# Kernel tuning notes

Hardware: AMD Instinct MI355X
Metric: run time of the kernel (lower is better)

The kernel has to match this reference:

```python
import jax, jax.numpy as jnp
import numpy as np

VOCAB = 65
N_EMBED = 384
BLOCK = 256
N_HEAD = 6
HEAD_SIZE = 4  # forward uses sa_heads = MultiHeadAttention(4), NOT the Block stack
B, T = 128, 256


def setup_inputs() -> dict:
    key = jax.random.key(0)
    ks = jax.random.split(key, 16)
    s = lambda *sh: 0.02
    inp = {
        "idx": jax.random.randint(ks[0], (B, T), 0, VOCAB),
        "targets": jax.random.randint(ks[1], (B, T), 0, VOCAB),
        "tok_emb": jax.random.normal(ks[2], (VOCAB, N_EMBED), jnp.float32) * 0.02,
        "pos_emb": jax.random.normal(ks[3], (BLOCK, N_EMBED), jnp.float32) * 0.02,
        "Wq": jax.random.normal(ks[4], (N_HEAD, N_EMBED, HEAD_SIZE), jnp.float32) * 0.05,
        "Wk": jax.random.normal(ks[5], (N_HEAD, N_EMBED, HEAD_SIZE), jnp.float32) * 0.05,
        "Wv": jax.random.normal(ks[6], (N_HEAD, N_EMBED, HEAD_SIZE), jnp.float32) * 0.05,
        "Wproj": jax.random.normal(ks[7], (N_HEAD * HEAD_SIZE, N_EMBED), jnp.float32) * 0.05,
        "bproj": jnp.zeros((N_EMBED,), jnp.float32),
        "W1": jax.random.normal(ks[8], (N_EMBED, 4 * N_EMBED), jnp.float32) * 0.02,
        "b1": jnp.zeros((4 * N_EMBED,), jnp.float32),
        "W2": jax.random.normal(ks[9], (4 * N_EMBED, N_EMBED), jnp.float32) * 0.02,
        "b2": jnp.zeros((N_EMBED,), jnp.float32),
        "Wlm": jax.random.normal(ks[10], (N_EMBED, VOCAB), jnp.float32) * 0.02,
        "blm": jnp.zeros((VOCAB,), jnp.float32),
    }
    return inp


def _forward(idx, targets, tok_emb, pos_emb, Wq, Wk, Wv, Wproj, bproj, W1, b1, W2, b2, Wlm, blm):
    Bb, Tt = idx.shape
    x = tok_emb[idx] + pos_emb[:Tt]  # [B,T,C]
    # multi-head attention (manual, causal). NOTE: source scales by n_embed**-0.5 (C of input), not head_size.
    q = jnp.einsum("btc,hcd->bhtd", x, Wq)
    k = jnp.einsum("btc,hcd->bhtd", x, Wk)
    v = jnp.einsum("btc,hcd->bhtd", x, Wv)
    scores = jnp.einsum("bhtd,bhsd->bhts", q, k) * (N_EMBED ** -0.5)
    causal = jnp.tril(jnp.ones((Tt, Tt), bool))
    scores = jnp.where(causal, scores, -jnp.inf)
    w = jax.nn.softmax(scores, axis=-1)  # dropout = identity in eval
    attn = jnp.einsum("bhts,bhsd->bhtd", w, v)
    attn = attn.transpose(0, 2, 1, 3).reshape(Bb, Tt, N_HEAD * HEAD_SIZE)
    x = attn @ Wproj + bproj
    # feed-forward
    x = jax.nn.relu(x @ W1 + b1) @ W2 + b2
    logits = x @ Wlm + blm  # [B,T,V]
    logits_flat = logits.reshape(Bb * Tt, VOCAB)
    t_flat = targets.reshape(Bb * Tt)
    logp = jax.nn.log_softmax(logits_flat, axis=-1)
    loss = -jnp.mean(jnp.take_along_axis(logp, t_flat[:, None], axis=1))
    return logits_flat, loss


def reference(idx, targets, tok_emb, pos_emb, Wq, Wk, Wv, Wproj, bproj, W1, b1, W2, b2, Wlm, blm):
    return _forward(idx, targets, tok_emb, pos_emb, Wq, Wk, Wv, Wproj, bproj, W1, b1, W2, b2, Wlm, blm)
```

## Files before the change

kernel.cpp:

```cpp
#include <hip/hip_runtime.h>
#include <hip/hip_bf16.h>
#include <math.h>

typedef __hip_bfloat16 bf16;
typedef __attribute__((ext_vector_type(8))) short bf16x8;
typedef __attribute__((ext_vector_type(4))) float f32x4;
typedef __attribute__((ext_vector_type(8))) int i32x8;
typedef __attribute__((ext_vector_type(4))) int i32x4;
typedef unsigned char u8;
typedef unsigned int u32;

#define T_SEQ   256
#define C_EMB   384
#define NH      6
#define HS      4
#define NB      128
#define NTOK    (NB * T_SEQ)
#define VOC     65
#define FFDIM   1536
#define QKVW    72
#define PROJK   32
#define XROWS   (VOC * T_SEQ)

#define X2_SCALE    128.0f
#define W1_SCALE    128.0f
#define FF1_DESCALE (1.0f / (128.0f * 128.0f))
#define H1_SCALE    512.0f
#define W2_SCALE    128.0f
#define FF2_DESCALE (1.0f / (512.0f * 128.0f))

__device__ __forceinline__ float b2f(bf16 x) { return __bfloat162float(x); }
__device__ __forceinline__ bf16  f2b(float x) { return __float2bfloat16(x); }
__device__ __forceinline__ short f2s(float x) { bf16 b = __float2bfloat16(x); return *reinterpret_cast<short*>(&b); }
__device__ __forceinline__ u8 f2fp8(float x) {
    return (u8)(__builtin_amdgcn_cvt_pk_fp8_f32(x, x, 0, false) & 0xff);
}
__device__ __forceinline__ u32 pk4fp8(const float* w) {
    int p = __builtin_amdgcn_cvt_pk_fp8_f32(w[0], w[1], 0, false);
    p = __builtin_amdgcn_cvt_pk_fp8_f32(w[2], w[3], p, true);
    return (u32)p;
}

__device__ __forceinline__ void glds16(const void* g, void* l) {
    __builtin_amdgcn_global_load_lds((const __attribute__((address_space(1))) void*)g,
                                     (__attribute__((address_space(3))) void*)l, 16, 0, 0);
}

__global__ void pack_all_kernel(const float* __restrict__ Wq, const float* __restrict__ Wk,
                                const float* __restrict__ Wv, const float* __restrict__ Wlm,
                                const float* __restrict__ Wproj,
                                const float* __restrict__ W1, const float* __restrict__ W2,
                                const float* __restrict__ tok_emb, const float* __restrict__ pos_emb,
                                bf16* __restrict__ WqkvT, bf16* __restrict__ WlmT,
                                bf16* __restrict__ WprojT, u8* __restrict__ W1f8,
                                u8* __restrict__ W2f8, bf16* __restrict__ xtab,
                                float* __restrict__ lossbuf) {
    int blk = blockIdx.x;
    if (blk == 0 && threadIdx.x == 0) { lossbuf[0] = 0.f; ((int*)lossbuf)[1] = 0; }
    if (blk < 128) {
        int n = blk;
        for (int c = threadIdx.x; c < C_EMB; c += 256) {
            float v = 0.f;
            if (n < QKVW) {
                int sel = n / 24, r = n % 24, h = r >> 2, d = r & 3;
                const float* W = (sel == 0) ? Wq : (sel == 1) ? Wk : Wv;
                v = W[(h * C_EMB + c) * HS + d];
            }
            WqkvT[(size_t)n * C_EMB + c] = f2b(v);
        }
    } else if (blk < 256) {
        int n = blk - 128;
        for (int c = threadIdx.x; c < C_EMB; c += 256)
            WlmT[(size_t)n * C_EMB + c] = f2b(n < VOC ? Wlm[(size_t)c * VOC + n] : 0.f);
    } else if (blk < 640) {
        int n = blk - 256;
        int k = threadIdx.x;
        if (k < PROJK)
            WprojT[(size_t)n * PROJK + k] = f2b(k < 24 ? Wproj[(size_t)k * C_EMB + n] : 0.f);
    } else if (blk < 640 + FFDIM) {
        int n = blk - 640;
        for (int k = threadIdx.x; k < C_EMB; k += 256)
            W1f8[(size_t)n * C_EMB + k] = f2fp8(W1[(size_t)k * FFDIM + n] * W1_SCALE);
    } else if (blk < 640 + FFDIM + C_EMB) {
        int n = blk - 640 - FFDIM;
        for (int k = threadIdx.x; k < FFDIM; k += 256)
            W2f8[(size_t)n * FFDIM + k] = f2fp8(W2[(size_t)k * C_EMB + n] * W2_SCALE);
    } else {
        int base = (blk - (640 + FFDIM + C_EMB)) * 4;
        for (int r = 0; r < 4; ++r) {
            int row = base + r;
            int id = row >> 8, t = row & 255;
            const float* te = tok_emb + (size_t)id * C_EMB;
            const float* pe = pos_emb + (size_t)t * C_EMB;
            bf16* dst = xtab + (size_t)row * C_EMB;
            for (int c = threadIdx.x; c < C_EMB; c += 256)
                dst[c] = f2b(te[c] + pe[c]);
        }
    }
}

__global__ __launch_bounds__(512)
void qkv_gather_kernel(const int* __restrict__ idx, const bf16* __restrict__ xtab,
                       const bf16* __restrict__ Bt, float* __restrict__ outf) {
    __shared__ __align__(16) u8 As[16384];
    __shared__ __align__(16) u8 Bs[16384];
    __shared__ int rowid[128];
    int tid = threadIdx.x, lane = tid & 63, wave = tid >> 6;
    int bm = blockIdx.x * 128;
    int wm = (wave & 1) * 64, wn = (wave >> 1) * 32;
    int lrow = lane & 15, kq = lane >> 4;
    if (tid < 128) { int token = bm + tid; rowid[tid] = idx[token] * T_SEQ + (token & (T_SEQ - 1)); }
    __syncthreads();

    int r0 = tid >> 3;
    int s0 = (((tid & 7) * 16) - (r0 & 7) * 16) & 127;
    int c1 = tid + 512;
    int r1 = c1 >> 3;
    int s1 = (((c1 & 7) * 16) - (r1 & 7) * 16) & 127;
    const u8* xb = (const u8*)xtab;
    const u8* bb = (const u8*)Bt;
    long gA0 = (long)rowid[r0] * 768 + s0;
    long gA1 = (long)rowid[r1] * 768 + s1;
    long gB0 = (long)r0 * 768 + s0;
    long gB1 = (long)r1 * 768 + s1;
    int ro = (lrow & 7) * 16;

    f32x4 acc[4][2] = {};
    for (int k0 = 0; k0 < 768; k0 += 128) {
        glds16(xb + gA0 + k0, As + (size_t)tid * 16);
        glds16(xb + gA1 + k0, As + (size_t)c1 * 16);
        glds16(bb + gB0 + k0, Bs + (size_t)tid * 16);
        glds16(bb + gB1 + k0, Bs + (size_t)c1 * 16);
        __syncthreads();
        #pragma unroll
        for (int ks = 0; ks < 2; ++ks) {
            int off = (ks * 64 + kq * 16 + ro) & 127;
            bf16x8 af[4], bff[2];
            #pragma unroll
            for (int i = 0; i < 4; ++i)
                af[i] = *(const bf16x8*)&As[(size_t)(wm + i * 16 + lrow) * 128 + off];
            #pragma unroll
            for (int i = 0; i < 2; ++i)
                bff[i] = *(const bf16x8*)&Bs[(size_t)(wn + i * 16 + lrow) * 128 + off];
            #pragma unroll
            for (int mi = 0; mi < 4; ++mi)
                #pragma unroll
                for (int ni = 0; ni < 2; ++ni)
                    acc[mi][ni] = __builtin_amdgcn_mfma_f32_16x16x32_bf16(af[mi], bff[ni], acc[mi][ni], 0, 0, 0);
        }
        __syncthreads();
    }

    #pragma unroll
    for (int ni = 0; ni < 2; ++ni) {
        int col = wn + ni * 16 + lrow;
        if (col >= QKVW) continue;
        #pragma unroll
        for (int mi = 0; mi < 4; ++mi) {
            int orow = bm + wm + mi * 16 + kq * 4;
            #pragma unroll
            for (int r = 0; r < 4; ++r)
                outf[(size_t)(orow + r) * QKVW + col] = acc[mi][ni][r];
        }
    }
}

__global__ void attn_kernel(const float* __restrict__ qkv,
                            bf16* __restrict__ attnT) {
    int bh = blockIdx.x;
    int b = bh / NH, h = bh % NH;
    int t = threadIdx.x;
    __shared__ float4 kv[T_SEQ][2];
    const float* base = qkv + (size_t)(b * T_SEQ) * QKVW;
    kv[t][0] = *(const float4*)(base + t * QKVW + 24 + h * HS);
    kv[t][1] = *(const float4*)(base + t * QKVW + 48 + h * HS);
    __syncthreads();
    const float scale = 0.05103103630798288f;
    float4 q = *(const float4*)(base + t * QKVW + h * HS);
    float qx = q.x * scale, qy = q.y * scale, qz = q.z * scale, qw = q.w * scale;
    float sum0 = 0.f, sum1 = 0.f;
    float o0x = 0.f, o0y = 0.f, o0z = 0.f, o0w = 0.f;
    float o1x = 0.f, o1y = 0.f, o1z = 0.f, o1w = 0.f;
    int s = 0;
    for (; s + 1 <= t; s += 2) {
        float4 k0 = kv[s][0],     v0 = kv[s][1];
        float4 k1 = kv[s + 1][0], v1 = kv[s + 1][1];
        float p0 = __expf(qx * k0.x + qy * k0.y + qz * k0.z + qw * k0.w);
        float p1 = __expf(qx * k1.x + qy * k1.y + qz * k1.z + qw * k1.w);
        sum0 += p0; sum1 += p1;
        o0x += p0 * v0.x; o0y += p0 * v0.y; o0z += p0 * v0.z; o0w += p0 * v0.w;
        o1x += p1 * v1.x; o1y += p1 * v1.y; o1z += p1 * v1.z; o1w += p1 * v1.w;
    }
    if (s <= t) {
        float4 k0 = kv[s][0], v0 = kv[s][1];
        float p0 = __expf(qx * k0.x + qy * k0.y + qz * k0.z + qw * k0.w);
        sum0 += p0;
        o0x += p0 * v0.x; o0y += p0 * v0.y; o0z += p0 * v0.z; o0w += p0 * v0.w;
    }
    float inv = 1.f / (sum0 + sum1);
    bf16* out = attnT + (size_t)(b * T_SEQ + t) * PROJK + h * HS;
    out[0] = f2b((o0x + o1x) * inv);
    out[1] = f2b((o0y + o1y) * inv);
    out[2] = f2b((o0z + o1z) * inv);
    out[3] = f2b((o0w + o1w) * inv);
    if (h == 0) {
        bf16* pad = attnT + (size_t)(b * T_SEQ + t) * PROJK + 24;
        *(uint4*)pad = uint4{0, 0, 0, 0};
    }
}

__global__ __launch_bounds__(256)
void gemm_mfma32_kernel(const bf16* __restrict__ A, const bf16* __restrict__ Bt,
                        const float* __restrict__ bias,
                        u8* __restrict__ outf8, float oscale,
                        int M, int K, int Nout) {
    __shared__ short As[128][32];
    __shared__ short Bs[128][32];
    int tid  = threadIdx.x;
    int lane = tid & 63;
    int wave = tid >> 6;
    int bm = blockIdx.y * 128;
    int bn = blockIdx.x * 128;
    int wm = (wave & 1) * 64;
    int wn = (wave >> 1) * 64;
    int lrow  = lane & 15;
    int khalf = lane >> 4;
    int arot = ((lrow >> 1) & 3) * 16;
    int roff = ((khalf * 16 + arot) & 63) >> 1;

    f32x4 acc[4][4] = {};
    for (int k0 = 0; k0 < K; k0 += 32) {
        #pragma unroll
        for (int h = 0; h < 2; ++h) {
            int c = tid + h * 256;
            int row = c >> 2;
            int i0 = (c & 3) * 16;
            int selem = ((i0 - ((row >> 1) & 3) * 16) & 63) >> 1;
            glds16(A  + (size_t)(bm + row) * K + k0 + selem, (short*)As + (size_t)c * 8);
            glds16(Bt + (size_t)(bn + row) * K + k0 + selem, (short*)Bs + (size_t)c * 8);
        }
        __syncthreads();

        bf16x8 af[4], bff[4];
        #pragma unroll
        for (int i = 0; i < 4; ++i) {
            af[i]  = *(const bf16x8*)&As[wm + i * 16 + lrow][roff];
            bff[i] = *(const bf16x8*)&Bs[wn + i * 16 + lrow][roff];
        }
        #pragma unroll
        for (int mi = 0; mi < 4; ++mi)
            #pragma unroll
            for (int ni = 0; ni < 4; ++ni)
                acc[mi][ni] = __builtin_amdgcn_mfma_f32_16x16x32_bf16(af[mi], bff[ni], acc[mi][ni], 0, 0, 0);
        __syncthreads();
    }

    #pragma unroll
    for (int ni = 0; ni < 4; ++ni) {
        int col = bn + wn + ni * 16 + lrow;
        float bv = bias[col];
        #pragma unroll
        for (int mi = 0; mi < 4; ++mi) {
            int row = bm + wm + mi * 16 + khalf * 4;
            float w[4];
            #pragma unroll
            for (int r = 0; r < 4; ++r) w[r] = (acc[mi][ni][r] + bv) * oscale;
            int p01 = __builtin_amdgcn_cvt_pk_fp8_f32(w[0], w[1], 0, false);
            int p23 = __builtin_amdgcn_cvt_pk_fp8_f32(w[2], w[3], 0, false);
            outf8[(size_t)(row + 0) * Nout + col] = (u8)(p01 & 0xff);
            outf8[(size_t)(row + 1) * Nout + col] = (u8)((p01 >> 8) & 0xff);
            outf8[(size_t)(row + 2) * Nout + col] = (u8)(p23 & 0xff);
            outf8[(size_t)(row + 3) * Nout + col] = (u8)((p23 >> 8) & 0xff);
        }
    }
}

__global__ __launch_bounds__(512)
void gemm_fp8_kernel(const u8* __restrict__ A, const u8* __restrict__ Bt,
                     const float* __restrict__ bias,
                     bf16* __restrict__ outb, u8* __restrict__ outf8,
                     float descale, float oscale,
                     int M, int K, int Nout, int NT, int relu) {
    __shared__ u8 smem[32768];
    u8* As = smem;
    u8* Bs = smem + 16384;
    int lin  = blockIdx.x;
    int xcd  = lin & 7;
    int loc  = lin >> 3;
    int nt   = loc % NT;
    int mloc = loc / NT;
    int MPX  = (M / 128) >> 3;
    int bm = (xcd * MPX + mloc) * 128;
    int bn = nt * 128;

    int tid  = threadIdx.x;
    int lane = tid & 63;
    int wave = tid >> 6;
    int wm = (wave & 1) * 64;
    int wn = (wave >> 1) * 32;
    int lrow  = lane & 15;
    int khalf = lane >> 4;

    f32x4 acc[4][2] = {};
    int r0 = tid >> 3;
    int i0 = (tid & 7) * 16;
    int s0 = (i0 - (r0 & 7) * 16) & 127;
    int arot = (lrow & 7) * 16;
    int off0 = (khalf * 32 + arot) & 127;
    int off1 = (off0 + 16) & 127;

    for (int k0 = 0; k0 < K; k0 += 128) {
        const u8* Ag = A  + (size_t)(bm + r0) * K + k0 + s0;
        const u8* Bg = Bt + (size_t)(bn + r0) * K + k0 + s0;
        glds16(Ag,                  As + (size_t)tid * 16);
        glds16(Ag + (size_t)64 * K, As + 8192 + (size_t)tid * 16);
        glds16(Bg,                  Bs + (size_t)tid * 16);
        glds16(Bg + (size_t)64 * K, Bs + 8192 + (size_t)tid * 16);
        __syncthreads();

        i32x8 a[4], b[2];
        #pragma unroll
        for (int i = 0; i < 4; ++i) {
            const u8* rp = As + (size_t)(wm + i * 16 + lrow) * 128;
            i32x4 lo = *(const i32x4*)(rp + off0);
            i32x4 hi = *(const i32x4*)(rp + off1);
            a[i][0]=lo[0]; a[i][1]=lo[1]; a[i][2]=lo[2]; a[i][3]=lo[3];
            a[i][4]=hi[0]; a[i][5]=hi[1]; a[i][6]=hi[2]; a[i][7]=hi[3];
        }
        #pragma unroll
        for (int i = 0; i < 2; ++i) {
            const u8* rp = Bs + (size_t)(wn + i * 16 + lrow) * 128;
            i32x4 lo = *(const i32x4*)(rp + off0);
            i32x4 hi = *(const i32x4*)(rp + off1);
            b[i][0]=lo[0]; b[i][1]=lo[1]; b[i][2]=lo[2]; b[i][3]=lo[3];
            b[i][4]=hi[0]; b[i][5]=hi[1]; b[i][6]=hi[2]; b[i][7]=hi[3];
        }
        #pragma unroll
        for (int mi = 0; mi < 4; ++mi)
            #pragma unroll
            for (int ni = 0; ni < 2; ++ni)
                acc[mi][ni] = __builtin_amdgcn_mfma_scale_f32_16x16x128_f8f6f4(
                    b[ni], a[mi], acc[mi][ni], 0, 0,
                    0, 0x7f7f7f7f, 0, 0x7f7f7f7f);
        __syncthreads();
    }

    if (outf8) {
        #pragma unroll
        for (int mi = 0; mi < 4; ++mi) {
            int m = wm + mi * 16 + lrow;
            #pragma unroll
            for (int ni = 0; ni < 2; ++ni) {
                int n0 = wn + ni * 16 + khalf * 4;
                float4 bv = *(const float4*)(bias + bn + n0);
                float w[4];
                w[0] = acc[mi][ni][0] * descale + bv.x;
                w[1] = acc[mi][ni][1] * descale + bv.y;
                w[2] = acc[mi][ni][2] * descale + bv.z;
                w[3] = acc[mi][ni][3] * descale + bv.w;
                if (relu) {
                    w[0] = fmaxf(w[0], 0.f); w[1] = fmaxf(w[1], 0.f);
                    w[2] = fmaxf(w[2], 0.f); w[3] = fmaxf(w[3], 0.f);
                }
                w[0] *= oscale; w[1] *= oscale; w[2] *= oscale; w[3] *= oscale;
                *(u32*)&smem[(size_t)m * 128 + ((n0 + (m & 7) * 16) & 127)] = pk4fp8(w);
            }
        }
        __syncthreads();
        #pragma unroll
        for (int p = 0; p < 2; ++p) {
            int c = tid + p * 512;
            int row = c >> 3;
            int g0 = (c & 7) * 16;
            uint4 v = *(const uint4*)&smem[(size_t)row * 128 + ((g0 + (row & 7) * 16) & 127)];
            *(uint4*)&outf8[(size_t)(bm + row) * Nout + bn + g0] = v;
        }
    } else {
        short* Es = (short*)smem;
        #pragma unroll
        for (int mi = 0; mi < 4; ++mi) {
            int m = wm + mi * 16 + lrow;
            #pragma unroll
            for (int ni = 0; ni < 2; ++ni) {
                int n0 = wn + ni * 16 + khalf * 4;
                float4 bv = *(const float4*)(bias + bn + n0);
                union { short s[4]; uint2 u; } pk;
                pk.s[0] = f2s(acc[mi][ni][0] * descale + bv.x);
                pk.s[1] = f2s(acc[mi][ni][1] * descale + bv.y);
                pk.s[2] = f2s(acc[mi][ni][2] * descale + bv.z);
                pk.s[3] = f2s(acc[mi][ni][3] * descale + bv.w);
                *(uint2*)&Es[(size_t)m * 128 + ((n0 + (m & 7) * 8) & 127)] = pk.u;
            }
        }
        __syncthreads();
        #pragma unroll
        for (int p = 0; p < 4; ++p) {
            int c = tid + p * 512;
            int row = c >> 4;
            int g0 = (c & 15) * 16;
            uint4 v = *(const uint4*)&smem[(size_t)row * 256 + ((g0 + (row & 7) * 16) & 255)];
            *(uint4*)((u8*)outb + ((size_t)(bm + row) * Nout + bn) * 2 + g0) = v;
        }
    }
}

__global__ __launch_bounds__(512)
void lm_loss_kernel(const bf16* __restrict__ A, const bf16* __restrict__ Bt,
                    const float* __restrict__ bias, const int* __restrict__ targets,
                    float* __restrict__ outf, float* __restrict__ lossbuf,
                    float* __restrict__ out_loss, int M, int K) {
    __shared__ short As[128][32];
    __shared__ short Bs[128][32];
    __shared__ float Ls[128][66];
    __shared__ float red[128];
    int tid  = threadIdx.x;
    int lane = tid & 63;
    int wave = tid >> 6;
    int bm = blockIdx.x * 128;
    int wm = (wave & 1) * 64;
    int wn = (wave >> 1) * 32;
    int lrow  = lane & 15;
    int khalf = lane >> 4;

    int row = tid >> 2;
    int i0 = (tid & 3) * 16;
    int selem = ((i0 - ((row >> 1) & 3) * 16) & 63) >> 1;
    int arot = ((lrow >> 1) & 3) * 16;
    int roff = ((khalf * 16 + arot) & 63) >> 1;

    f32x4 acc[4][2] = {};
    for (int k0 = 0; k0 < K; k0 += 32) {
        glds16(A  + (size_t)(bm + row) * K + k0 + selem, (short*)As + (size_t)tid * 8);
        glds16(Bt + (size_t)row * K + k0 + selem,        (short*)Bs + (size_t)tid * 8);
        __syncthreads();

        bf16x8 af[4], bff[2];
        #pragma unroll
        for (int i = 0; i < 4; ++i)
            af[i] = *(const bf16x8*)&As[wm + i * 16 + lrow][roff];
        #pragma unroll
        for (int i = 0; i < 2; ++i)
            bff[i] = *(const bf16x8*)&Bs[wn + i * 16 + lrow][roff];
        #pragma unroll
        for (int mi = 0; mi < 4; ++mi)
            #pragma unroll
            for (int ni = 0; ni < 2; ++ni)
                acc[mi][ni] = __builtin_amdgcn_mfma_f32_16x16x32_bf16(af[mi], bff[ni], acc[mi][ni], 0, 0, 0);
        __syncthreads();
    }

    #pragma unroll
    for (int ni = 0; ni < 2; ++ni) {
        int col = wn + ni * 16 + lrow;
        if (col >= VOC) continue;
        float bv = bias[col];
        #pragma unroll
        for (int mi = 0; mi < 4; ++mi) {
            int lr = wm + mi * 16 + khalf * 4;
            #pragma unroll
            for (int r = 0; r < 4; ++r) {
                float v = acc[mi][ni][r] + bv;
                outf[(size_t)(bm + lr + r) * VOC + col] = v;
                Ls[lr + r][col] = v;
            }
        }
    }
    __syncthreads();

    if (tid < 128) {
        int token = bm + tid;
        int tgt = targets[token];
        float m = -1e30f, s = 0.f;
        #pragma unroll 8
        for (int c = 0; c < VOC; ++c) {
            float v = Ls[tid][c];
            float mn = fmaxf(m, v);
            s = s * __expf(m - mn) + __expf(v - mn);
            m = mn;
        }
        red[tid] = m + logf(s) - Ls[tid][tgt];
    }
    __syncthreads();
    if (tid < 64) {
        float s = red[tid] + red[tid + 64];
        #pragma unroll
        for (int off = 32; off > 0; off >>= 1) s += __shfl_xor(s, off);
        if (tid == 0) {
            atomicAdd(&lossbuf[0], s);
            __threadfence();
            int done = atomicAdd(&((int*)lossbuf)[1], 1);
            if (done == (NTOK / 128) - 1) {
                __threadfence();
                float total = atomicAdd(&lossbuf[0], 0.0f);
                out_loss[0] = total / (float)NTOK;
            }
        }
    }
}

extern "C" void kernel_launch(void* const* d_in, const int* in_sizes, int n_in,
                              void* d_out, int out_size, void* d_ws, size_t ws_size,
                              hipStream_t stream) {
    const int*   idx     = (const int*)  d_in[0];
    const int*   targets = (const int*)  d_in[1];
    const float* tok_emb = (const float*)d_in[2];
    const float* pos_emb = (const float*)d_in[3];
    const float* Wq      = (const float*)d_in[4];
    const float* Wk      = (const float*)d_in[5];
    const float* Wv      = (const float*)d_in[6];
    const float* Wproj   = (const float*)d_in[7];
    const float* bproj   = (const float*)d_in[8];
    const float* W1      = (const float*)d_in[9];
    const float* b1      = (const float*)d_in[10];
    const float* W2      = (const float*)d_in[11];
    const float* b2      = (const float*)d_in[12];
    const float* Wlm     = (const float*)d_in[13];
    const float* blm     = (const float*)d_in[14];

    char* ws = (char*)d_ws;
    bf16*  WprojT = (bf16*) (ws + 0);
    float* qkvbuf = (float*)(ws + 25165824);
    bf16*  attnT  = (bf16*) (ws + 34603008);
    bf16*  xtab   = (bf16*) (ws + 37748736);
    u8*    h1f8   = (u8*)   (ws + 62914560);
    u8*    x2f8   = (u8*)   (ws + 113246208);
    bf16*  x3     = (bf16*) (ws + 163577856);
    float* lossbuf= (float*)(ws + 188743680);
    u8*    W1f8   = (u8*)   (ws + 188874752);
    u8*    W2f8   = (u8*)   (ws + 190054400);
    bf16*  WqkvT  = (bf16*) (ws + 191234048);
    bf16*  WlmT   = (bf16*) (ws + 191332352);

    float* out_logits = (float*)d_out;
    float* out_loss   = out_logits + (size_t)NTOK * VOC;

    pack_all_kernel<<<640 + FFDIM + C_EMB + XROWS / 4, 256, 0, stream>>>(
        Wq, Wk, Wv, Wlm, Wproj, W1, W2, tok_emb, pos_emb,
        WqkvT, WlmT, WprojT, W1f8, W2f8, xtab, lossbuf);

    qkv_gather_kernel<<<NTOK / 128, 512, 0, stream>>>(idx, xtab, WqkvT, qkvbuf);
    attn_kernel<<<NB * NH, T_SEQ, 0, stream>>>(qkvbuf, attnT);

    gemm_mfma32_kernel<<<dim3(C_EMB / 128, NTOK / 128), 256, 0, stream>>>(attnT, WprojT, bproj,
                                                                          x2f8, X2_SCALE,
                                                                          NTOK, PROJK, C_EMB);
    gemm_fp8_kernel<<<(NTOK / 128) * (FFDIM / 128), 512, 0, stream>>>(x2f8, W1f8, b1,
                                                                      nullptr, h1f8,
                                                                      FF1_DESCALE, H1_SCALE,
                                                                      NTOK, C_EMB, FFDIM, FFDIM / 128, 1);
    gemm_fp8_kernel<<<(NTOK / 128) * (C_EMB / 128), 512, 0, stream>>>(h1f8, W2f8, b2,
                                                                      x3, nullptr,
                                                                      FF2_DESCALE, 1.0f,
                                                                      NTOK, FFDIM, C_EMB, C_EMB / 128, 0);
    lm_loss_kernel<<<NTOK / 128, 512, 0, stream>>>(x3, WlmT, blm, targets,
                                                   out_logits, lossbuf, out_loss, NTOK, C_EMB);
}
```

Measured before the change: 228.3 us.

## Fuse projection, FF1 and FF2 GEMMs into one per-tile kernel

New measurement: 210.0 us. 8.0% less time.

```diff
diff --git a/kernel.cpp b/kernel.cpp
--- a/kernel.cpp
+++ b/kernel.cpp
@@ -29,7 +29,7 @@
 #define W2_SCALE    128.0f
 #define FF2_DESCALE (1.0f / (512.0f * 128.0f))
 
-__device__ __forceinline__ float b2f(bf16 x) { return __bfloat162float(x); }
+__device__ __forceinline__ float bf2f(bf16 x) { return __bfloat162float(x); }
 __device__ __forceinline__ bf16  f2b(float x) { return __float2bfloat16(x); }
 __device__ __forceinline__ short f2s(float x) { bf16 b = __float2bfloat16(x); return *reinterpret_cast<short*>(&b); }
 __device__ __forceinline__ u8 f2fp8(float x) {
@@ -209,198 +209,232 @@
     }
 }
 
-__global__ __launch_bounds__(256)
-void gemm_mfma32_kernel(const bf16* __restrict__ A, const bf16* __restrict__ Bt,
-                        const float* __restrict__ bias,
-                        u8* __restrict__ outf8, float oscale,
-                        int M, int K, int Nout) {
-    __shared__ short As[128][32];
-    __shared__ short Bs[128][32];
+__global__ __launch_bounds__(512, 2)
+void ff_mega_kernel(const bf16* __restrict__ attnT, const bf16* __restrict__ WprojT,
+                    const float* __restrict__ bproj,
+                    const u8* __restrict__ W1f8, const float* __restrict__ b1,
+                    const u8* __restrict__ W2f8, const float* __restrict__ b2,
+                    bf16* __restrict__ x3) {
+    __shared__ __align__(16) u8 smem[147456];
+    u8* x2_lds = smem;
+    u8* bs1    = smem + 49152;
+    u8* h1t    = smem + 81920;
+    u8* bs2    = smem + 98304;
+    short* As_p = (short*)(smem + 49152);
+    short* Bs_p = (short*)(smem + 57344);
+
     int tid  = threadIdx.x;
     int lane = tid & 63;
     int wave = tid >> 6;
-    int bm = blockIdx.y * 128;
-    int bn = blockIdx.x * 128;
-    int wm = (wave & 1) * 64;
-    int wn = (wave >> 1) * 64;
+    int bm   = blockIdx.x * 128;
+    int wm   = (wave & 1) * 64;
     int lrow  = lane & 15;
     int khalf = lane >> 4;
-    int arot = ((lrow >> 1) & 3) * 16;
-    int roff = ((khalf * 16 + arot) & 63) >> 1;
-
-    f32x4 acc[4][4] = {};
-    for (int k0 = 0; k0 < K; k0 += 32) {
-        #pragma unroll
-        for (int h = 0; h < 2; ++h) {
-            int c = tid + h * 256;
-            int row = c >> 2;
-            int i0 = (c & 3) * 16;
-            int selem = ((i0 - ((row >> 1) & 3) * 16) & 63) >> 1;
-            glds16(A  + (size_t)(bm + row) * K + k0 + selem, (short*)As + (size_t)c * 8);
-            glds16(Bt + (size_t)(bn + row) * K + k0 + selem, (short*)Bs + (size_t)c * 8);
-        }
-        __syncthreads();
-
-        bf16x8 af[4], bff[4];
-        #pragma unroll
-        for (int i = 0; i < 4; ++i) {
-            af[i]  = *(const bf16x8*)&As[wm + i * 16 + lrow][roff];
-            bff[i] = *(const bf16x8*)&Bs[wn + i * 16 + lrow][roff];
-        }
+
+    {
+        int row = tid >> 2;
+        int i0 = (tid & 3) * 16;
+        int selem = ((i0 - ((row >> 1) & 3) * 16) & 63) >> 1;
+        glds16(attnT + (size_t)(bm + row) * PROJK + selem, As_p + (size_t)tid * 8);
+        #pragma unroll
+        for (int p = 0; p < 3; ++p) {
+            int c = tid + p * 512;
+            int rowb = c >> 2;
+            int sel2 = (((c & 3) * 16 - ((rowb >> 1) & 3) * 16) & 63) >> 1;
+            glds16(WprojT + (size_t)rowb * PROJK + sel2, Bs_p + (size_t)c * 8);
+        }
+    }
+    __syncthreads();
+
+    int wn6 = (wave >> 1) * 96;
+    f32x4 accp[4][6] = {};
+    {
+        int arot16 = ((lrow >> 1) & 3) * 16;
+        int roff = ((khalf * 16 + arot16) & 63) >> 1;
+        bf16x8 afp[4], bfp[6];
+        #pragma unroll
+        for (int i = 0; i < 4; ++i)
+            afp[i] = *(const bf16x8*)&As_p[(size_t)(wm + i * 16 + lrow) * 32 + roff];
+        #pragma unroll
+        for (int i = 0; i < 6; ++i)
+            bfp[i] = *(const bf16x8*)&Bs_p[(size_t)(wn6 + i * 16 + lrow) * 32 + roff];
         #pragma unroll
         for (int mi = 0; mi < 4; ++mi)
             #pragma unroll
-            for (int ni = 0; ni < 4; ++ni)
-                acc[mi][ni] = __builtin_amdgcn_mfma_f32_16x16x32_bf16(af[mi], bff[ni], acc[mi][ni], 0, 0, 0);
-        __syncthreads();
+            for (int ni = 0; ni < 6; ++ni)
+                accp[mi][ni] = __builtin_amdgcn_mfma_f32_16x16x32_bf16(bfp[ni], afp[mi], accp[mi][ni], 0, 0, 0);
+    }
+    __syncthreads();
+
+    int r0 = tid >> 3;
+    int s0 = (((tid & 7) * 16) - (r0 & 7) * 16) & 127;
+
+    {
+        const u8* g = W1f8 + (size_t)r0 * 384 + s0;
+        glds16(g, bs1 + (size_t)tid * 16);
+        glds16(g + (size_t)64 * 384, bs1 + 8192 + (size_t)tid * 16);
+        const u8* g2 = W2f8 + (size_t)r0 * 1536 + s0;
+        #pragma unroll
+        for (int j = 0; j < 6; ++j)
+            glds16(g2 + (size_t)j * 64 * 1536, bs2 + (size_t)j * 8192 + (size_t)tid * 16);
     }
 
     #pragma unroll
-    for (int ni = 0; ni < 4; ++ni) {
-        int col = bn + wn + ni * 16 + lrow;
-        float bv = bias[col];
-        #pragma unroll
-        for (int mi = 0; mi < 4; ++mi) {
-            int row = bm + wm + mi * 16 + khalf * 4;
+    for (int mi = 0; mi < 4; ++mi) {
+        int m = wm + mi * 16 + lrow;
+        #pragma unroll
+        for (int ni = 0; ni < 6; ++ni) {
+            int n0 = wn6 + ni * 16 + khalf * 4;
+            float4 bv = *(const float4*)(bproj + n0);
             float w[4];
-            #pragma unroll
-            for (int r = 0; r < 4; ++r) w[r] = (acc[mi][ni][r] + bv) * oscale;
-            int p01 = __builtin_amdgcn_cvt_pk_fp8_f32(w[0], w[1], 0, false);
-            int p23 = __builtin_amdgcn_cvt_pk_fp8_f32(w[2], w[3], 0, false);
-            outf8[(size_t)(row + 0) * Nout + col] = (u8)(p01 & 0xff);
-            outf8[(size_t)(row + 1) * Nout + col] = (u8)((p01 >> 8) & 0xff);
-            outf8[(size_t)(row + 2) * Nout + col] = (u8)(p23 & 0xff);
-            outf8[(size_t)(row + 3) * Nout + col] = (u8)((p23 >> 8) & 0xff);
-        }
-    }
-}
-
-__global__ __launch_bounds__(512)
-void gemm_fp8_kernel(const u8* __restrict__ A, const u8* __restrict__ Bt,
-                     const float* __restrict__ bias,
-                     bf16* __restrict__ outb, u8* __restrict__ outf8,
-                     float descale, float oscale,
-                     int M, int K, int Nout, int NT, int relu) {
-    __shared__ u8 smem[32768];
-    u8* As = smem;
-    u8* Bs = smem + 16384;
-    int lin  = blockIdx.x;
-    int xcd  = lin & 7;
-    int loc  = lin >> 3;
-    int nt   = loc % NT;
-    int mloc = loc / NT;
-    int MPX  = (M / 128) >> 3;
-    int bm = (xcd * MPX + mloc) * 128;
-    int bn = nt * 128;
-
-    int tid  = threadIdx.x;
-    int lane = tid & 63;
-    int wave = tid >> 6;
-    int wm = (wave & 1) * 64;
-    int wn = (wave >> 1) * 32;
-    int lrow  = lane & 15;
-    int khalf = lane >> 4;
-
-    f32x4 acc[4][2] = {};
-    int r0 = tid >> 3;
-    int i0 = (tid & 7) * 16;
-    int s0 = (i0 - (r0 & 7) * 16) & 127;
-    int arot = (lrow & 7) * 16;
-    int off0 = (khalf * 32 + arot) & 127;
+            w[0] = (accp[mi][ni][0] + bv.x) * X2_SCALE;
+            w[1] = (accp[mi][ni][1] + bv.y) * X2_SCALE;
+            w[2] = (accp[mi][ni][2] + bv.z) * X2_SCALE;
+            w[3] = (accp[mi][ni][3] + bv.w) * X2_SCALE;
+            *(u32*)&x2_lds[(size_t)(n0 >> 7) * 16384 + (size_t)m * 128 +
+                           (((n0 & 127) + (m & 7) * 16) & 127)] = pk4fp8(w);
+        }
+    }
+    __syncthreads();
+
+    int arot8 = (lrow & 7) * 16;
+    int off0 = (khalf * 32 + arot8) & 127;
     int off1 = (off0 + 16) & 127;
-
-    for (int k0 = 0; k0 < K; k0 += 128) {
-        const u8* Ag = A  + (size_t)(bm + r0) * K + k0 + s0;
-        const u8* Bg = Bt + (size_t)(bn + r0) * K + k0 + s0;
-        glds16(Ag,                  As + (size_t)tid * 16);
-        glds16(Ag + (size_t)64 * K, As + 8192 + (size_t)tid * 16);
-        glds16(Bg,                  Bs + (size_t)tid * 16);
-        glds16(Bg + (size_t)64 * K, Bs + 8192 + (size_t)tid * 16);
-        __syncthreads();
-
-        i32x8 a[4], b[2];
-        #pragma unroll
-        for (int i = 0; i < 4; ++i) {
-            const u8* rp = As + (size_t)(wm + i * 16 + lrow) * 128;
-            i32x4 lo = *(const i32x4*)(rp + off0);
-            i32x4 hi = *(const i32x4*)(rp + off1);
-            a[i][0]=lo[0]; a[i][1]=lo[1]; a[i][2]=lo[2]; a[i][3]=lo[3];
-            a[i][4]=hi[0]; a[i][5]=hi[1]; a[i][6]=hi[2]; a[i][7]=hi[3];
-        }
-        #pragma unroll
-        for (int i = 0; i < 2; ++i) {
-            const u8* rp = Bs + (size_t)(wn + i * 16 + lrow) * 128;
-            i32x4 lo = *(const i32x4*)(rp + off0);
-            i32x4 hi = *(const i32x4*)(rp + off1);
-            b[i][0]=lo[0]; b[i][1]=lo[1]; b[i][2]=lo[2]; b[i][3]=lo[3];
-            b[i][4]=hi[0]; b[i][5]=hi[1]; b[i][6]=hi[2]; b[i][7]=hi[3];
-        }
-        #pragma unroll
-        for (int mi = 0; mi < 4; ++mi)
-            #pragma unroll
-            for (int ni = 0; ni < 2; ++ni)
-                acc[mi][ni] = __builtin_amdgcn_mfma_scale_f32_16x16x128_f8f6f4(
-                    b[ni], a[mi], acc[mi][ni], 0, 0,
-                    0, 0x7f7f7f7f, 0, 0x7f7f7f7f);
-        __syncthreads();
-    }
-
-    if (outf8) {
+    int wn2 = (wave >> 1) * 32;
+
+    f32x4 acc1[4][2] = {};
+    f32x4 acc2[4][6] = {};
+
+    for (int nt = 0; nt < 12; ++nt) {
+        #pragma unroll
+        for (int kk = 0; kk < 3; ++kk) {
+            int stp = nt * 3 + kk;
+            int cur = stp & 1;
+            int nxt = stp + 1;
+            if (nxt < 36) {
+                int nnt = nxt / 3, nk0 = (nxt % 3) * 128;
+                const u8* g = W1f8 + (size_t)(nnt * 128 + r0) * 384 + nk0 + s0;
+                u8* dst = bs1 + (size_t)(nxt & 1) * 16384;
+                glds16(g, dst + (size_t)tid * 16);
+                glds16(g + (size_t)64 * 384, dst + 8192 + (size_t)tid * 16);
+            }
+            const u8* abase = x2_lds + (size_t)kk * 16384;
+            const u8* bbase = bs1 + (size_t)cur * 16384;
+            i32x8 a[4], b[2];
+            #pragma unroll
+            for (int i = 0; i < 4; ++i) {
+                const u8* rp = abase + (size_t)(wm + i * 16 + lrow) * 128;
+                i32x4 lo = *(const i32x4*)(rp + off0);
+                i32x4 hi = *(const i32x4*)(rp + off1);
+                a[i][0]=lo[0]; a[i][1]=lo[1]; a[i][2]=lo[2]; a[i][3]=lo[3];
+                a[i][4]=hi[0]; a[i][5]=hi[1]; a[i][6]=hi[2]; a[i][7]=hi[3];
+            }
+            #pragma unroll
+            for (int i = 0; i < 2; ++i) {
+                const u8* rp = bbase + (size_t)(wn2 + i * 16 + lrow) * 128;
+                i32x4 lo = *(const i32x4*)(rp + off0);
+                i32x4 hi = *(const i32x4*)(rp + off1);
+                b[i][0]=lo[0]; b[i][1]=lo[1]; b[i][2]=lo[2]; b[i][3]=lo[3];
+                b[i][4]=hi[0]; b[i][5]=hi[1]; b[i][6]=hi[2]; b[i][7]=hi[3];
+            }
+            #pragma unroll
+            for (int mi = 0; mi < 4; ++mi)
+                #pragma unroll
+                for (int ni = 0; ni < 2; ++ni)
+                    acc1[mi][ni] = __builtin_amdgcn_mfma_scale_f32_16x16x128_f8f6f4(
+                        b[ni], a[mi], acc1[mi][ni], 0, 0,
+                        0, 0x7f7f7f7f, 0, 0x7f7f7f7f);
+            __syncthreads();
+        }
+
         #pragma unroll
         for (int mi = 0; mi < 4; ++mi) {
             int m = wm + mi * 16 + lrow;
             #pragma unroll
             for (int ni = 0; ni < 2; ++ni) {
-                int n0 = wn + ni * 16 + khalf * 4;
-                float4 bv = *(const float4*)(bias + bn + n0);
+                int n0 = wn2 + ni * 16 + khalf * 4;
+                float4 bv = *(const float4*)(b1 + nt * 128 + n0);
                 float w[4];
-                w[0] = acc[mi][ni][0] * descale + bv.x;
-                w[1] = acc[mi][ni][1] * descale + bv.y;
-                w[2] = acc[mi][ni][2] * descale + bv.z;
-                w[3] = acc[mi][ni][3] * descale + bv.w;
-                if (relu) {
-                    w[0] = fmaxf(w[0], 0.f); w[1] = fmaxf(w[1], 0.f);
-                    w[2] = fmaxf(w[2], 0.f); w[3] = fmaxf(w[3], 0.f);
+                w[0] = fmaxf(acc1[mi][ni][0] * FF1_DESCALE + bv.x, 0.f) * H1_SCALE;
+                w[1] = fmaxf(acc1[mi][ni][1] * FF1_DESCALE + bv.y, 0.f) * H1_SCALE;
+                w[2] = fmaxf(acc1[mi][ni][2] * FF1_DESCALE + bv.z, 0.f) * H1_SCALE;
+                w[3] = fmaxf(acc1[mi][ni][3] * FF1_DESCALE + bv.w, 0.f) * H1_SCALE;
+                *(u32*)&h1t[(size_t)m * 128 + ((n0 + (m & 7) * 16) & 127)] = pk4fp8(w);
+                acc1[mi][ni] = f32x4{0.f, 0.f, 0.f, 0.f};
+            }
+        }
+        __syncthreads();
+
+        {
+            i32x8 a2[4];
+            #pragma unroll
+            for (int i = 0; i < 4; ++i) {
+                const u8* rp = h1t + (size_t)(wm + i * 16 + lrow) * 128;
+                i32x4 lo = *(const i32x4*)(rp + off0);
+                i32x4 hi = *(const i32x4*)(rp + off1);
+                a2[i][0]=lo[0]; a2[i][1]=lo[1]; a2[i][2]=lo[2]; a2[i][3]=lo[3];
+                a2[i][4]=hi[0]; a2[i][5]=hi[1]; a2[i][6]=hi[2]; a2[i][7]=hi[3];
+            }
+            #pragma unroll
+            for (int half = 0; half < 2; ++half) {
+                i32x8 bw[3];
+                #pragma unroll
+                for (int j = 0; j < 3; ++j) {
+                    int ni = half * 3 + j;
+                    const u8* rp = bs2 + (size_t)(wn6 + ni * 16 + lrow) * 128;
+                    i32x4 lo = *(const i32x4*)(rp + off0);
+                    i32x4 hi = *(const i32x4*)(rp + off1);
+                    bw[j][0]=lo[0]; bw[j][1]=lo[1]; bw[j][2]=lo[2]; bw[j][3]=lo[3];
+                    bw[j][4]=hi[0]; bw[j][5]=hi[1]; bw[j][6]=hi[2]; bw[j][7]=hi[3];
                 }
-                w[0] *= oscale; w[1] *= oscale; w[2] *= oscale; w[3] *= oscale;
-                *(u32*)&smem[(size_t)m * 128 + ((n0 + (m & 7) * 16) & 127)] = pk4fp8(w);
+                #pragma unroll
+                for (int mi = 0; mi < 4; ++mi)
+                    #pragma unroll
+                    for (int j = 0; j < 3; ++j)
+                        acc2[mi][half * 3 + j] = __builtin_amdgcn_mfma_scale_f32_16x16x128_f8f6f4(
+                            bw[j], a2[mi], acc2[mi][half * 3 + j], 0, 0,
+                            0, 0x7f7f7f7f, 0, 0x7f7f7f7f);
             }
         }
         __syncthreads();
-        #pragma unroll
-        for (int p = 0; p < 2; ++p) {
-            int c = tid + p * 512;
-            int row = c >> 3;
-            int g0 = (c & 7) * 16;
-            uint4 v = *(const uint4*)&smem[(size_t)row * 128 + ((g0 + (row & 7) * 16) & 127)];
-            *(uint4*)&outf8[(size_t)(bm + row) * Nout + bn + g0] = v;
-        }
-    } else {
-        short* Es = (short*)smem;
-        #pragma unroll
-        for (int mi = 0; mi < 4; ++mi) {
-            int m = wm + mi * 16 + lrow;
-            #pragma unroll
-            for (int ni = 0; ni < 2; ++ni) {
-                int n0 = wn + ni * 16 + khalf * 4;
-                float4 bv = *(const float4*)(bias + bn + n0);
-                union { short s[4]; uint2 u; } pk;
-                pk.s[0] = f2s(acc[mi][ni][0] * descale + bv.x);
-                pk.s[1] = f2s(acc[mi][ni][1] * descale + bv.y);
-                pk.s[2] = f2s(acc[mi][ni][2] * descale + bv.z);
-                pk.s[3] = f2s(acc[mi][ni][3] * descale + bv.w);
-                *(uint2*)&Es[(size_t)m * 128 + ((n0 + (m & 7) * 8) & 127)] = pk.u;
-            }
-        }
-        __syncthreads();
-        #pragma unroll
-        for (int p = 0; p < 4; ++p) {
-            int c = tid + p * 512;
-            int row = c >> 4;
-            int g0 = (c & 15) * 16;
-            uint4 v = *(const uint4*)&smem[(size_t)row * 256 + ((g0 + (row & 7) * 16) & 255)];
-            *(uint4*)((u8*)outb + ((size_t)(bm + row) * Nout + bn) * 2 + g0) = v;
-        }
+
+        if (nt + 1 < 12) {
+            const u8* g2 = W2f8 + (size_t)r0 * 1536 + (nt + 1) * 128 + s0;
+            #pragma unroll
+            for (int j = 0; j < 6; ++j)
+                glds16(g2 + (size_t)j * 64 * 1536, bs2 + (size_t)j * 8192 + (size_t)tid * 16);
+        }
+    }
+
+    u8* Ep = smem;
+    #pragma unroll
+    for (int mi = 0; mi < 4; ++mi) {
+        int m = wm + mi * 16 + lrow;
+        #pragma unroll
+        for (int ni = 0; ni < 6; ++ni) {
+            int n0 = wn6 + ni * 16 + khalf * 4;
+            float4 bv = *(const float4*)(b2 + n0);
+            union { short s[4]; uint2 u; } pk;
+            pk.s[0] = f2s(acc2[mi][ni][0] * FF2_DESCALE + bv.x);
+            pk.s[1] = f2s(acc2[mi][ni][1] * FF2_DESCALE + bv.y);
+            pk.s[2] = f2s(acc2[mi][ni][2] * FF2_DESCALE + bv.z);
+            pk.s[3] = f2s(acc2[mi][ni][3] * FF2_DESCALE + bv.w);
+            *(uint2*)&Ep[(size_t)m * 768 + ((n0 >> 7) << 8) +
+                         ((((n0 & 127) * 2) + (m & 7) * 16) & 255)] = pk.u;
+        }
+    }
+    __syncthreads();
+    #pragma unroll
+    for (int p = 0; p < 12; ++p) {
+        int c = tid + p * 512;
+        int row = c / 48;
+        int sl = c - row * 48;
+        int g0 = sl * 16;
+        int chunk = g0 >> 8;
+        int loc = g0 & 255;
+        uint4 v = *(const uint4*)&Ep[(size_t)row * 768 + (chunk << 8) +
+                                     ((loc + (row & 7) * 16) & 255)];
+        *(uint4*)((u8*)x3 + (size_t)(bm + row) * 768 + g0) = v;
     }
 }
 
@@ -522,8 +556,6 @@
     float* qkvbuf = (float*)(ws + 25165824);
     bf16*  attnT  = (bf16*) (ws + 34603008);
     bf16*  xtab   = (bf16*) (ws + 37748736);
-    u8*    h1f8   = (u8*)   (ws + 62914560);
-    u8*    x2f8   = (u8*)   (ws + 113246208);
     bf16*  x3     = (bf16*) (ws + 163577856);
     float* lossbuf= (float*)(ws + 188743680);
     u8*    W1f8   = (u8*)   (ws + 188874752);
@@ -541,17 +573,9 @@
     qkv_gather_kernel<<<NTOK / 128, 512, 0, stream>>>(idx, xtab, WqkvT, qkvbuf);
     attn_kernel<<<NB * NH, T_SEQ, 0, stream>>>(qkvbuf, attnT);
 
-    gemm_mfma32_kernel<<<dim3(C_EMB / 128, NTOK / 128), 256, 0, stream>>>(attnT, WprojT, bproj,
-                                                                          x2f8, X2_SCALE,
-                                                                          NTOK, PROJK, C_EMB);
-    gemm_fp8_kernel<<<(NTOK / 128) * (FFDIM / 128), 512, 0, stream>>>(x2f8, W1f8, b1,
-                                                                      nullptr, h1f8,
-                                                                      FF1_DESCALE, H1_SCALE,
-                                                                      NTOK, C_EMB, FFDIM, FFDIM / 128, 1);
-    gemm_fp8_kernel<<<(NTOK / 128) * (C_EMB / 128), 512, 0, stream>>>(h1f8, W2f8, b2,
-                                                                      x3, nullptr,
-                                                                      FF2_DESCALE, 1.0f,
-                                                                      NTOK, FFDIM, C_EMB, C_EMB / 128, 0);
+    ff_mega_kernel<<<NTOK / 128, 512, 0, stream>>>(attnT, WprojT, bproj,
+                                                   W1f8, b1, W2f8, b2, x3);
+
     lm_loss_kernel<<<NTOK / 128, 512, 0, stream>>>(x3, WlmT, blm, targets,
                                                    out_logits, lossbuf, out_loss, NTOK, C_EMB);
 }
```

## Fuse attention projection into FF1 GEMM with x2 kept in LDS

Applied to the files above, without the earlier changes.

After: 231.9 us. No clear change (+1.6%).

```diff
diff --git a/kernel.cpp b/kernel.cpp
--- a/kernel.cpp
+++ b/kernel.cpp
@@ -29,7 +29,7 @@
 #define W2_SCALE    128.0f
 #define FF2_DESCALE (1.0f / (512.0f * 128.0f))
 
-__device__ __forceinline__ float b2f(bf16 x) { return __bfloat162float(x); }
+__device__ __forceinline__ float bf2f(bf16 x) { return __bfloat162float(x); }
 __device__ __forceinline__ bf16  f2b(float x) { return __float2bfloat16(x); }
 __device__ __forceinline__ short f2s(float x) { bf16 b = __float2bfloat16(x); return *reinterpret_cast<short*>(&b); }
 __device__ __forceinline__ u8 f2fp8(float x) {
@@ -52,14 +52,15 @@
                                 const float* __restrict__ W1, const float* __restrict__ W2,
                                 const float* __restrict__ tok_emb, const float* __restrict__ pos_emb,
                                 bf16* __restrict__ WqkvT, bf16* __restrict__ WlmT,
-                                bf16* __restrict__ WprojT, u8* __restrict__ W1f8,
+                                bf16* __restrict__ WprojT, u8* __restrict__ W1P,
                                 u8* __restrict__ W2f8, bf16* __restrict__ xtab,
                                 float* __restrict__ lossbuf) {
     int blk = blockIdx.x;
-    if (blk == 0 && threadIdx.x == 0) { lossbuf[0] = 0.f; ((int*)lossbuf)[1] = 0; }
+    int t = threadIdx.x;
+    if (blk == 0 && t == 0) { lossbuf[0] = 0.f; ((int*)lossbuf)[1] = 0; }
     if (blk < 128) {
         int n = blk;
-        for (int c = threadIdx.x; c < C_EMB; c += 256) {
+        for (int c = t; c < C_EMB; c += 256) {
             float v = 0.f;
             if (n < QKVW) {
                 int sel = n / 24, r = n % 24, h = r >> 2, d = r & 3;
@@ -70,30 +71,39 @@
         }
     } else if (blk < 256) {
         int n = blk - 128;
-        for (int c = threadIdx.x; c < C_EMB; c += 256)
+        for (int c = t; c < C_EMB; c += 256)
             WlmT[(size_t)n * C_EMB + c] = f2b(n < VOC ? Wlm[(size_t)c * VOC + n] : 0.f);
     } else if (blk < 640) {
         int n = blk - 256;
-        int k = threadIdx.x;
+        int k = t;
         if (k < PROJK)
             WprojT[(size_t)n * PROJK + k] = f2b(k < 24 ? Wproj[(size_t)k * C_EMB + n] : 0.f);
-    } else if (blk < 640 + FFDIM) {
-        int n = blk - 640;
-        for (int k = threadIdx.x; k < C_EMB; k += 256)
-            W1f8[(size_t)n * C_EMB + k] = f2fp8(W1[(size_t)k * FFDIM + n] * W1_SCALE);
-    } else if (blk < 640 + FFDIM + C_EMB) {
-        int n = blk - 640 - FFDIM;
-        for (int k = threadIdx.x; k < FFDIM; k += 256)
+    } else if (blk < 640 + 288) {
+        int fb = blk - 640;
+        int n16 = fb / 3, kk = fb % 3;
+        int b0 = t * 8;
+        int l = b0 >> 5;
+        int j0 = b0 & 31;
+        int n = n16 * 16 + (l & 15);
+        int kb = kk * 128 + (l >> 4) * 32 + j0;
+        union { u8 b[8]; uint2 u; } pk;
+        #pragma unroll
+        for (int e = 0; e < 8; ++e)
+            pk.b[e] = f2fp8(W1[(size_t)(kb + e) * FFDIM + n] * W1_SCALE);
+        *(uint2*)&W1P[(size_t)fb * 2048 + b0] = pk.u;
+    } else if (blk < 640 + 288 + 384) {
+        int n = blk - 928;
+        for (int k = t; k < FFDIM; k += 256)
             W2f8[(size_t)n * FFDIM + k] = f2fp8(W2[(size_t)k * C_EMB + n] * W2_SCALE);
     } else {
-        int base = (blk - (640 + FFDIM + C_EMB)) * 4;
+        int base = (blk - 1312) * 4;
         for (int r = 0; r < 4; ++r) {
             int row = base + r;
-            int id = row >> 8, t = row & 255;
+            int id = row >> 8, tt = row & 255;
             const float* te = tok_emb + (size_t)id * C_EMB;
-            const float* pe = pos_emb + (size_t)t * C_EMB;
+            const float* pe = pos_emb + (size_t)tt * C_EMB;
             bf16* dst = xtab + (size_t)row * C_EMB;
-            for (int c = threadIdx.x; c < C_EMB; c += 256)
+            for (int c = t; c < C_EMB; c += 256)
                 dst[c] = f2b(te[c] + pe[c]);
         }
     }
@@ -209,69 +219,143 @@
     }
 }
 
-__global__ __launch_bounds__(256)
-void gemm_mfma32_kernel(const bf16* __restrict__ A, const bf16* __restrict__ Bt,
-                        const float* __restrict__ bias,
-                        u8* __restrict__ outf8, float oscale,
-                        int M, int K, int Nout) {
-    __shared__ short As[128][32];
-    __shared__ short Bs[128][32];
+__global__ __launch_bounds__(512, 2)
+void ff1_kernel(const bf16* __restrict__ attnT, const bf16* __restrict__ WprojT,
+                const float* __restrict__ bproj,
+                const u8* __restrict__ W1P, const float* __restrict__ b1,
+                u8* __restrict__ h1f8) {
+    __shared__ __align__(16) u8 smem[81920];
+    u8* x2_lds = smem;
+    u8* h1s    = smem + 49152;
+    short* As_p = (short*)(smem + 49152);
+    short* Bs_p = (short*)(smem + 57344);
+
     int tid  = threadIdx.x;
     int lane = tid & 63;
     int wave = tid >> 6;
-    int bm = blockIdx.y * 128;
-    int bn = blockIdx.x * 128;
-    int wm = (wave & 1) * 64;
-    int wn = (wave >> 1) * 64;
+    int bm   = blockIdx.x * 128;
     int lrow  = lane & 15;
     int khalf = lane >> 4;
-    int arot = ((lrow >> 1) & 3) * 16;
-    int roff = ((khalf * 16 + arot) & 63) >> 1;
-
-    f32x4 acc[4][4] = {};
-    for (int k0 = 0; k0 < K; k0 += 32) {
-        #pragma unroll
-        for (int h = 0; h < 2; ++h) {
-            int c = tid + h * 256;
-            int row = c >> 2;
-            int i0 = (c & 3) * 16;
-            int selem = ((i0 - ((row >> 1) & 3) * 16) & 63) >> 1;
-            glds16(A  + (size_t)(bm + row) * K + k0 + selem, (short*)As + (size_t)c * 8);
-            glds16(Bt + (size_t)(bn + row) * K + k0 + selem, (short*)Bs + (size_t)c * 8);
-        }
-        __syncthreads();
-
-        bf16x8 af[4], bff[4];
-        #pragma unroll
-        for (int i = 0; i < 4; ++i) {
-            af[i]  = *(const bf16x8*)&As[wm + i * 16 + lrow][roff];
-            bff[i] = *(const bf16x8*)&Bs[wn + i * 16 + lrow][roff];
-        }
-        #pragma unroll
-        for (int mi = 0; mi < 4; ++mi)
-            #pragma unroll
-            for (int ni = 0; ni < 4; ++ni)
-                acc[mi][ni] = __builtin_amdgcn_mfma_f32_16x16x32_bf16(af[mi], bff[ni], acc[mi][ni], 0, 0, 0);
-        __syncthreads();
-    }
-
-    #pragma unroll
-    for (int ni = 0; ni < 4; ++ni) {
-        int col = bn + wn + ni * 16 + lrow;
-        float bv = bias[col];
-        #pragma unroll
-        for (int mi = 0; mi < 4; ++mi) {
-            int row = bm + wm + mi * 16 + khalf * 4;
-            float w[4];
-            #pragma unroll
-            for (int r = 0; r < 4; ++r) w[r] = (acc[mi][ni][r] + bv) * oscale;
-            int p01 = __builtin_amdgcn_cvt_pk_fp8_f32(w[0], w[1], 0, false);
-            int p23 = __builtin_amdgcn_cvt_pk_fp8_f32(w[2], w[3], 0, false);
-            outf8[(size_t)(row + 0) * Nout + col] = (u8)(p01 & 0xff);
-            outf8[(size_t)(row + 1) * Nout + col] = (u8)((p01 >> 8) & 0xff);
-            outf8[(size_t)(row + 2) * Nout + col] = (u8)(p23 & 0xff);
-            outf8[(size_t)(row + 3) * Nout + col] = (u8)((p23 >> 8) & 0xff);
-        }
+
+    {
+        int row = tid >> 2;
+        int i0 = (tid & 3) * 16;
+        int selem = ((i0 - ((row >> 1) & 3) * 16) & 63) >> 1;
+        glds16(attnT + (size_t)(bm + row) * PROJK + selem, As_p + (size_t)tid * 8);
+        #pragma unroll
+        for (int p = 0; p < 3; ++p) {
+            int c = tid + p * 512;
+            int rowb = c >> 2;
+            int sel2 = (((c & 3) * 16 - ((rowb >> 1) & 3) * 16) & 63) >> 1;
+            glds16(WprojT + (size_t)rowb * PROJK + sel2, Bs_p + (size_t)c * 8);
+        }
+    }
+    __syncthreads();
+
+    {
+        int wmP = (wave & 1) * 64;
+        int wn6 = (wave >> 1) * 96;
+        int arot16 = ((lrow >> 1) & 3) * 16;
+        int roff = ((khalf * 16 + arot16) & 63) >> 1;
+        #pragma unroll
+        for (int ph = 0; ph < 2; ++ph) {
+            f32x4 accp[4][3] = {};
+            bf16x8 afp[4], bfp[3];
+            #pragma unroll
+            for (int i = 0; i < 4; ++i)
+                afp[i] = *(const bf16x8*)&As_p[(size_t)(wmP + i * 16 + lrow) * 32 + roff];
+            #pragma unroll
+            for (int i = 0; i < 3; ++i)
+                bfp[i] = *(const bf16x8*)&Bs_p[(size_t)(wn6 + (ph * 3 + i) * 16 + lrow) * 32 + roff];
+            #pragma unroll
+            for (int mi = 0; mi < 4; ++mi)
+                #pragma unroll
+                for (int ni = 0; ni < 3; ++ni)
+                    accp[mi][ni] = __builtin_amdgcn_mfma_f32_16x16x32_bf16(bfp[ni], afp[mi], accp[mi][ni], 0, 0, 0);
+            #pragma unroll
+            for (int mi = 0; mi < 4; ++mi) {
+                int m = wmP + mi * 16 + lrow;
+                #pragma unroll
+                for (int ni = 0; ni < 3; ++ni) {
+                    int n0 = wn6 + (ph * 3 + ni) * 16 + khalf * 4;
+                    float4 bv = *(const float4*)(bproj + n0);
+                    float w[4];
+                    w[0] = (accp[mi][ni][0] + bv.x) * X2_SCALE;
+                    w[1] = (accp[mi][ni][1] + bv.y) * X2_SCALE;
+                    w[2] = (accp[mi][ni][2] + bv.z) * X2_SCALE;
+                    w[3] = (accp[mi][ni][3] + bv.w) * X2_SCALE;
+                    *(u32*)&x2_lds[(size_t)(n0 >> 7) * 16384 + (size_t)m * 128 +
+                                   (((n0 & 127) + (m & 7) * 16) & 127)] = pk4fp8(w);
+                }
+            }
+        }
+    }
+    __syncthreads();
+
+    int wm1 = (wave & 3) * 32;
+    int wc  = wave >> 2;
+    int arot8 = (lrow & 7) * 16;
+    int off0 = (khalf * 32 + arot8) & 127;
+    int off1 = (off0 + 16) & 127;
+
+    for (int nt = 0; nt < 6; ++nt) {
+        f32x4 acc1[2][8] = {};
+        #pragma unroll
+        for (int kk = 0; kk < 3; ++kk) {
+            const u8* abase = x2_lds + (size_t)kk * 16384;
+            i32x8 a[2];
+            #pragma unroll
+            for (int i = 0; i < 2; ++i) {
+                const u8* rp = abase + (size_t)(wm1 + i * 16 + lrow) * 128;
+                i32x4 lo = *(const i32x4*)(rp + off0);
+                i32x4 hi = *(const i32x4*)(rp + off1);
+                a[i][0]=lo[0]; a[i][1]=lo[1]; a[i][2]=lo[2]; a[i][3]=lo[3];
+                a[i][4]=hi[0]; a[i][5]=hi[1]; a[i][6]=hi[2]; a[i][7]=hi[3];
+            }
+            const u8* wbase = W1P + ((size_t)((nt * 16 + wc * 8) * 3 + kk)) * 2048
+                                  + (size_t)lane * 32;
+            #pragma unroll
+            for (int j = 0; j < 8; ++j) {
+                const u8* p = wbase + (size_t)j * 3 * 2048;
+                i32x4 lo = *(const i32x4*)p;
+                i32x4 hi = *(const i32x4*)(p + 16);
+                i32x8 b;
+                b[0]=lo[0]; b[1]=lo[1]; b[2]=lo[2]; b[3]=lo[3];
+                b[4]=hi[0]; b[5]=hi[1]; b[6]=hi[2]; b[7]=hi[3];
+                #pragma unroll
+                for (int mi = 0; mi < 2; ++mi)
+                    acc1[mi][j] = __builtin_amdgcn_mfma_scale_f32_16x16x128_f8f6f4(
+                        b, a[mi], acc1[mi][j], 0, 0,
+                        0, 0x7f7f7f7f, 0, 0x7f7f7f7f);
+            }
+        }
+
+        #pragma unroll
+        for (int mi = 0; mi < 2; ++mi) {
+            int m = wm1 + mi * 16 + lrow;
+            #pragma unroll
+            for (int ni = 0; ni < 8; ++ni) {
+                int n0 = wc * 128 + ni * 16 + khalf * 4;
+                float4 bv = *(const float4*)(b1 + nt * 256 + n0);
+                float w[4];
+                w[0] = fmaxf(acc1[mi][ni][0] * FF1_DESCALE + bv.x, 0.f) * H1_SCALE;
+                w[1] = fmaxf(acc1[mi][ni][1] * FF1_DESCALE + bv.y, 0.f) * H1_SCALE;
+                w[2] = fmaxf(acc1[mi][ni][2] * FF1_DESCALE + bv.z, 0.f) * H1_SCALE;
+                w[3] = fmaxf(acc1[mi][ni][3] * FF1_DESCALE + bv.w, 0.f) * H1_SCALE;
+                *(u32*)&h1s[(size_t)m * 256 + ((n0 + (m & 7) * 16) & 255)] = pk4fp8(w);
+            }
+        }
+        __syncthreads();
+
+        #pragma unroll
+        for (int p = 0; p < 4; ++p) {
+            int c = tid + p * 512;
+            int row = c >> 4;
+            int g0 = (c & 15) * 16;
+            uint4 v = *(const uint4*)&h1s[(size_t)row * 256 + ((g0 + (row & 7) * 16) & 255)];
+            *(uint4*)&h1f8[(size_t)(bm + row) * FFDIM + nt * 256 + g0] = v;
+        }
+        __syncthreads();
     }
 }
 
@@ -523,10 +607,9 @@
     bf16*  attnT  = (bf16*) (ws + 34603008);
     bf16*  xtab   = (bf16*) (ws + 37748736);
     u8*    h1f8   = (u8*)   (ws + 62914560);
-    u8*    x2f8   = (u8*)   (ws + 113246208);
     bf16*  x3     = (bf16*) (ws + 163577856);
     float* lossbuf= (float*)(ws + 188743680);
-    u8*    W1f8   = (u8*)   (ws + 188874752);
+    u8*    W1P    = (u8*)   (ws + 188874752);
     u8*    W2f8   = (u8*)   (ws + 190054400);
     bf16*  WqkvT  = (bf16*) (ws + 191234048);
     bf16*  WlmT   = (bf16*) (ws + 191332352);
@@ -534,24 +617,20 @@
     float* out_logits = (float*)d_out;
     float* out_loss   = out_logits + (size_t)NTOK * VOC;
 
-    pack_all_kernel<<<640 + FFDIM + C_EMB + XROWS / 4, 256, 0, stream>>>(
+    pack_all_kernel<<<1312 + XROWS / 4, 256, 0, stream>>>(
         Wq, Wk, Wv, Wlm, Wproj, W1, W2, tok_emb, pos_emb,
-        WqkvT, WlmT, WprojT, W1f8, W2f8, xtab, lossbuf);
+        WqkvT, WlmT, WprojT, W1P, W2f8, xtab, lossbuf);
 
     qkv_gather_kernel<<<NTOK / 128, 512, 0, stream>>>(idx, xtab, WqkvT, qkvbuf);
     attn_kernel<<<NB * NH, T_SEQ, 0, stream>>>(qkvbuf, attnT);
 
-    gemm_mfma32_kernel<<<dim3(C_EMB / 128, NTOK / 128), 256, 0, stream>>>(attnT, WprojT, bproj,
-                                                                          x2f8, X2_SCALE,
-                                                                          NTOK, PROJK, C_EMB);
-    gemm_fp8_kernel<<<(NTOK / 128) * (FFDIM / 128), 512, 0, stream>>>(x2f8, W1f8, b1,
-                                                                      nullptr, h1f8,
-                                                                      FF1_DESCALE, H1_SCALE,
-                                                                      NTOK, C_EMB, FFDIM, FFDIM / 128, 1);
+    ff1_kernel<<<NTOK / 128, 512, 0, stream>>>(attnT, WprojT, bproj, W1P, b1, h1f8);
+
     gemm_fp8_kernel<<<(NTOK / 128) * (C_EMB / 128), 512, 0, stream>>>(h1f8, W2f8, b2,
                                                                       x3, nullptr,
                                                                       FF2_DESCALE, 1.0f,
                                                                       NTOK, FFDIM, C_EMB, C_EMB / 128, 0);
+
     lm_loss_kernel<<<NTOK / 128, 512, 0, stream>>>(x3, WlmT, blm, targets,
                                                    out_logits, lossbuf, out_loss, NTOK, C_EMB);
 }
```
